# Performance work log

Measured on AMD Instinct MI355X. Metric: run time of the kernel, lower is better.

Reference implementation:

```python
import jax, jax.numpy as jnp
import numpy as np
from jax import lax

# Hyperparameters (match init_kwargs)
B, DIM, H, W = 8, 384, 32, 32
HEADS = 8
GROUPS = 4
OFF_SCALE = 4
K1, K2 = 5, 11  # generate_offset_kernel_sizes(4) -> [5, 11]
OFF_DIM = DIM // GROUPS  # 96
HEAD_DIM = DIM // HEADS  # 48
DN = ('NCHW', 'OIHW', 'NCHW')


def setup_inputs() -> dict:
    key = jax.random.key(0)
    ks = jax.random.split(key, 9)
    std = 0.02
    return {
        'x': jax.random.normal(ks[0], (B, DIM, H, W), jnp.float32),
        'Wq': jax.random.normal(ks[1], (DIM, DIM), jnp.float32) * std,
        'Wk': jax.random.normal(ks[2], (DIM, DIM), jnp.float32) * std,
        'Wv': jax.random.normal(ks[3], (DIM, DIM), jnp.float32) * std,
        'Wproj': jax.random.normal(ks[4], (DIM, DIM), jnp.float32) * std,
        'bproj': jnp.zeros((DIM,), jnp.float32),
        'scale': jnp.ones((1, HEADS, 1, 1), jnp.float32) / np.sqrt(HEAD_DIM),
        'Woff1': jax.random.normal(ks[5], (2, OFF_DIM, K1, K1), jnp.float32) * std,
        'Woff2': jax.random.normal(ks[6], (2, OFF_DIM, K2, K2), jnp.float32) * std,
    }


def _group(t, b, h, w):
    # 'b (h w) (g c) -> (b g) c h w'
    cg = t.shape[-1] // GROUPS
    return t.reshape(b, h, w, GROUPS, cg).transpose(0, 3, 4, 1, 2).reshape(b * GROUPS, cg, h, w)


def _ungroup(t, b, h, w):
    # '(b g) c h w -> b (h w) (g c)'
    cg = t.shape[1]
    return t.reshape(b, GROUPS, cg, h, w).transpose(0, 3, 4, 1, 2).reshape(b, h * w, GROUPS * cg)


def _bilinear(img, ys, xs):
    # img: (c, h, w); ys, xs: (h, w) absolute pixel coords -> (c, h, w)
    h, w = img.shape[1], img.shape[2]
    ys = jnp.clip(ys, 0.0, h - 1.0)
    xs = jnp.clip(xs, 0.0, w - 1.0)
    y0 = jnp.floor(ys); x0 = jnp.floor(xs)
    y0i = y0.astype(jnp.int32); x0i = x0.astype(jnp.int32)
    y1i = jnp.minimum(y0i + 1, h - 1); x1i = jnp.minimum(x0i + 1, w - 1)
    wy = ys - y0; wx = xs - x0
    g = lambda yi, xi: img[:, yi, xi]  # (c, h, w) gather
    return (g(y0i, x0i) * (1 - wy) * (1 - wx) + g(y0i, x1i) * (1 - wy) * wx
            + g(y1i, x0i) * wy * (1 - wx) + g(y1i, x1i) * wy * wx)


def reference(x, Wq, Wk, Wv, Wproj, bproj, scale, Woff1, Woff2):
    b, c, h, w = x.shape
    n = h * w
    xt = x.reshape(b, c, n).transpose(0, 2, 1)  # b n c
    q = xt @ Wq.T  # b n c

    # Offset generator: per-group multi-scale convs -> tanh-bounded offsets scaled by offset_scale
    qg = _group(q, b, h, w)  # (b*g, off_dim, h, w)
    off = (lax.conv_general_dilated(qg, Woff1, (1, 1), 'SAME', dimension_numbers=DN)
           + lax.conv_general_dilated(qg, Woff2, (1, 1), 'SAME', dimension_numbers=DN))
    offsets = jnp.tanh(off) * OFF_SCALE  # (b*g, 2, h, w)

    # apply_offsets: bilinear gather of grouped x at base grid + offsets
    xg = _group(xt, b, h, w)  # (b*g, off_dim, h, w)
    by, bx = jnp.meshgrid(jnp.arange(h, dtype=jnp.float32), jnp.arange(w, dtype=jnp.float32), indexing='ij')
    ys = by[None] + offsets[:, 0]
    xs = bx[None] + offsets[:, 1]
    kv = jax.vmap(_bilinear)(xg, ys, xs)  # (b*g, off_dim, h, w)
    kvf = _ungroup(kv, b, h, w)  # b n c

    k = kvf @ Wk.T
    v = kvf @ Wv.T
    heads = lambda t: t.reshape(b, n, HEADS, HEAD_DIM).transpose(0, 2, 1, 3)  # b h n d
    qh, kh, vh = heads(q), heads(k), heads(v)

    attn = jnp.einsum('bhid,bhjd->bhij', qh, kh) * scale  # learnable per-head scale
    attn = jax.nn.softmax(attn, axis=-1)
    out = jnp.einsum('bhij,bhjd->bhid', attn, vh)  # b h n d
    out = out.transpose(0, 2, 1, 3).reshape(b, n, c)
    out = out @ Wproj.T + bproj
    return out.transpose(0, 2, 1).reshape(b, c, h, w)
```

## Files before the change

### kernel.cpp

```cpp
#include <hip/hip_runtime.h>
#include <hip/hip_bf16.h>

#define DIMC 384
#define NHEADS 8
#define HDIM 48
#define OFFD 96
#define NPIX 1024
#define BB 8

typedef short bf16s;
typedef __attribute__((ext_vector_type(8))) short short8;
typedef __attribute__((ext_vector_type(4))) float f32x4;

__device__ __forceinline__ short f2b(float f) {
  union { float f; unsigned u; } v; v.f = f;
  unsigned r = (v.u + 0x7fffu + ((v.u >> 16) & 1u)) >> 16;
  return (short)r;
}
__device__ __forceinline__ float b2f(short s) {
  union { unsigned u; float f; } v; v.u = ((unsigned)(unsigned short)s) << 16; return v.f;
}
__device__ __forceinline__ unsigned pk2(float a, float b) {
  union { __hip_bfloat162 h; unsigned u; } v;
  v.h = __float22bfloat162_rn(float2{a, b});
  return v.u;
}

__global__ __launch_bounds__(256) void prep_weights(
    const float* __restrict__ Wq, const float* __restrict__ Wk,
    const float* __restrict__ Wv, const float* __restrict__ Wp,
    bf16s* __restrict__ wqh, bf16s* __restrict__ wql,
    bf16s* __restrict__ wkb, bf16s* __restrict__ wvb, bf16s* __restrict__ wpb) {
  int idx = blockIdx.x * 256 + threadIdx.x;
  if (idx >= 4 * 147456) return;
  int which = idx / 147456, e = idx % 147456;
  if (which == 0) {
    float v = Wq[e]; short h = f2b(v);
    wqh[e] = h; wql[e] = f2b(v - b2f(h));
  } else if (which == 1) wkb[e] = f2b(Wk[e]);
  else if (which == 2) wvb[e] = f2b(Wv[e]);
  else wpb[e] = f2b(Wp[e]);
}

__global__ __launch_bounds__(256) void transpose_split(const float* __restrict__ x,
    bf16s* __restrict__ xh, bf16s* __restrict__ xl) {
  __shared__ float ts[64][65];
  int np0 = blockIdx.x * 64, c0 = blockIdx.y * 64, b = blockIdx.z;
  int t = threadIdx.x;
  int a = t & 63, bq = t >> 6;
#pragma unroll
  for (int i = 0; i < 16; ++i) {
    int cl = bq + i * 4;
    ts[cl][a] = x[((size_t)(b * DIMC + c0 + cl)) * NPIX + np0 + a];
  }
  __syncthreads();
#pragma unroll
  for (int i = 0; i < 16; ++i) {
    int npl = bq + i * 4;
    float v = ts[a][npl];
    short h = f2b(v);
    size_t o = ((size_t)(b * NPIX + np0 + npl)) * DIMC + c0 + a;
    xh[o] = h; xl[o] = f2b(v - b2f(h));
  }
}

template<int MODE>
__global__ __launch_bounds__(256) void gemm_lds(
    const bf16s* __restrict__ Ah, const bf16s* __restrict__ Al,
    const bf16s* __restrict__ Wa, const bf16s* __restrict__ Wb,
    float* __restrict__ outF, bf16s* __restrict__ outB, bf16s* __restrict__ outB2,
    const float* __restrict__ bias) {
  __shared__ __align__(16) short wlds[25600];
  const int NS  = (MODE == 2) ? 1 : 2;
  const int KCN = (MODE == 2) ? 48 : 24;
  const int STR = (MODE == 2) ? 392 : 200;
  int t = threadIdx.x;
  int w = t >> 6, lane = t & 63, quad = lane >> 4, l16 = lane & 15;
  int n0 = blockIdx.x * 64;
  int m0 = blockIdx.y * 64 + w * 16;
  f32x4 acc[4], acc2[4];
#pragma unroll
  for (int nt = 0; nt < 4; ++nt) {
    acc[nt] = (f32x4){0.f, 0.f, 0.f, 0.f};
    if (MODE != 2) acc2[nt] = (f32x4){0.f, 0.f, 0.f, 0.f};
  }
  const bf16s* arow_a = Ah + (size_t)(m0 + l16) * DIMC;
  const bf16s* arow_l = (MODE == 0) ? (Al + (size_t)(m0 + l16) * DIMC) : nullptr;

  for (int s = 0; s < NS; ++s) {
    if (s) __syncthreads();
    int kcb = s * 24;
#pragma unroll
    for (int ii = 0; ii < (KCN * 64) / 256; ++ii) {
      int i = ii * 256 + t;
      int n = i / KCN, kcl = i % KCN;
      *(short8*)(&wlds[n * STR + kcl * 8]) =
          *(const short8*)(Wa + (size_t)(n0 + n) * DIMC + (kcb + kcl) * 8);
      if (MODE != 2)
        *(short8*)(&wlds[12800 + n * STR + kcl * 8]) =
            *(const short8*)(Wb + (size_t)(n0 + n) * DIMC + (kcb + kcl) * 8);
    }
    __syncthreads();
    int k0beg = s * 6, k0cnt = (MODE == 2) ? 12 : 6;
#pragma unroll
    for (int kk = 0; kk < k0cnt; ++kk) {
      int k0 = k0beg + kk;
      short8 a0 = *(const short8*)(arow_a + k0 * 32 + quad * 8);
      short8 a1;
      if (MODE == 0) a1 = *(const short8*)(arow_l + k0 * 32 + quad * 8);
      int kcl = kk * 4 + quad;
#pragma unroll
      for (int nt = 0; nt < 4; ++nt) {
        int n = nt * 16 + l16;
        short8 b0 = *(const short8*)(&wlds[n * STR + kcl * 8]);
        acc[nt] = __builtin_amdgcn_mfma_f32_16x16x32_bf16(a0, b0, acc[nt], 0, 0, 0);
        if (MODE == 0) {
          short8 b1 = *(const short8*)(&wlds[12800 + n * STR + kcl * 8]);
          acc[nt] = __builtin_amdgcn_mfma_f32_16x16x32_bf16(a1, b0, acc[nt], 0, 0, 0);
          acc[nt] = __builtin_amdgcn_mfma_f32_16x16x32_bf16(a0, b1, acc[nt], 0, 0, 0);
        } else if (MODE == 1) {
          short8 b1 = *(const short8*)(&wlds[12800 + n * STR + kcl * 8]);
          acc2[nt] = __builtin_amdgcn_mfma_f32_16x16x32_bf16(a0, b1, acc2[nt], 0, 0, 0);
        }
      }
    }
  }
#pragma unroll
  for (int nt = 0; nt < 4; ++nt) {
    int c = n0 + nt * 16 + l16;
#pragma unroll
    for (int r = 0; r < 4; ++r) {
      int m = m0 + quad * 4 + r;
      int b = m >> 10, np = m & 1023;
      float v = acc[nt][r];
      if (MODE == 0) {
        int g = c / OFFD, cc = c % OFFD;
        outF[((size_t)((b * 4 + g) * OFFD + cc)) * NPIX + np] = v;
        int h = c / HDIM, d = c % HDIM;
        outB[((size_t)((b * 8 + h) * NPIX + np)) * 64 + d] = f2b(v);
      } else if (MODE == 1) {
        int h = c / HDIM, d = c % HDIM;
        outB[((size_t)((b * 8 + h) * NPIX + np)) * 64 + d] = f2b(v);
        outB2[((size_t)((b * 8 + h) * HDIM + d)) * NPIX + np] = f2b(acc2[nt][r]);
      } else {
        outF[((size_t)(b * DIMC + c)) * NPIX + np] = v + bias[c];
      }
    }
  }
}

__global__ __launch_bounds__(256) void conv_off_part(const float* __restrict__ qg,
    const float* __restrict__ W1, const float* __restrict__ W2, float* __restrict__ pbuf) {
  __shared__ float ts[42 * 43];
  int chunk = blockIdx.x & 15, bg = blockIdx.x >> 4;
  int t = threadIdx.x;
  int y = t >> 3, x0 = (t & 7) * 4;
  float a0[4] = {0.f, 0.f, 0.f, 0.f}, a1[4] = {0.f, 0.f, 0.f, 0.f};
  const float* plane0 = qg + (size_t)bg * OFFD * NPIX;
  for (int ci = 0; ci < 6; ++ci) {
    int cc = chunk * 6 + ci;
    const float* plane = plane0 + (size_t)cc * NPIX;
    __syncthreads();
    for (int e = t; e < 42 * 42; e += 256) {
      int r = e / 42, c = e - r * 42;
      int gy = r - 5, gx = c - 5;
      ts[r * 43 + c] = (gy >= 0 && gy < 32 && gx >= 0 && gx < 32) ? plane[gy * 32 + gx] : 0.f;
    }
    __syncthreads();
    const float* w1c0 = W1 + (size_t)cc * 25;
    const float* w1c1 = W1 + (size_t)(OFFD + cc) * 25;
    const float* w2c0 = W2 + (size_t)cc * 121;
    const float* w2c1 = W2 + (size_t)(OFFD + cc) * 121;
#pragma unroll
    for (int ky = 0; ky < 11; ++ky) {
      float rv[14];
#pragma unroll
      for (int j = 0; j < 14; ++j) rv[j] = ts[(y + ky) * 43 + x0 + j];
#pragma unroll
      for (int kx = 0; kx < 11; ++kx) {
        float w0 = w2c0[ky * 11 + kx], w1v = w2c1[ky * 11 + kx];
#pragma unroll
        for (int o = 0; o < 4; ++o) {
          a0[o] = fmaf(rv[kx + o], w0, a0[o]);
          a1[o] = fmaf(rv[kx + o], w1v, a1[o]);
        }
      }
    }
#pragma unroll
    for (int ky = 0; ky < 5; ++ky) {
      float rv[8];
#pragma unroll
      for (int j = 0; j < 8; ++j) rv[j] = ts[(y + ky + 3) * 43 + x0 + 3 + j];
#pragma unroll
      for (int kx = 0; kx < 5; ++kx) {
        float w0 = w1c0[ky * 5 + kx], w1v = w1c1[ky * 5 + kx];
#pragma unroll
        for (int o = 0; o < 4; ++o) {
          a0[o] = fmaf(rv[kx + o], w0, a0[o]);
          a1[o] = fmaf(rv[kx + o], w1v, a1[o]);
        }
      }
    }
  }
  float* pb = pbuf + ((size_t)(chunk * 32 + bg) * 2) * NPIX;
#pragma unroll
  for (int o = 0; o < 4; ++o) {
    int n = y * 32 + x0 + o;
    pb[n] = a0[o];
    pb[NPIX + n] = a1[o];
  }
}

__global__ __launch_bounds__(256) void conv_off_reduce(const float* __restrict__ pbuf,
                                                       float* __restrict__ offs) {
  int idx = blockIdx.x * 256 + threadIdx.x;
  float s = 0.f;
#pragma unroll
  for (int ch = 0; ch < 16; ++ch) s += pbuf[(size_t)ch * 65536 + idx];
  offs[idx] = tanhf(s) * 4.0f;
}

__global__ __launch_bounds__(256) void bilinear_kernel(const float* __restrict__ x,
    const float* __restrict__ offs, bf16s* __restrict__ kvf) {
  int chunk = blockIdx.x & 7, ntile = (blockIdx.x >> 3) & 3, bg = blockIdx.x >> 5;
  int n = ntile * 256 + threadIdx.x;
  int b = bg >> 2, g = bg & 3;
  int iy = n >> 5, ix = n & 31;
  float ys = (float)iy + offs[(size_t)bg * 2 * NPIX + n];
  float xs = (float)ix + offs[(size_t)bg * 2 * NPIX + NPIX + n];
  ys = fminf(fmaxf(ys, 0.f), 31.f);
  xs = fminf(fmaxf(xs, 0.f), 31.f);
  float y0f = floorf(ys), x0f = floorf(xs);
  int y0 = (int)y0f, x0 = (int)x0f;
  int y1 = min(y0 + 1, 31), x1 = min(x0 + 1, 31);
  float wy = ys - y0f, wx = xs - x0f;
  float w00 = (1.f - wy) * (1.f - wx), w01 = (1.f - wy) * wx;
  float w10 = wy * (1.f - wx), w11 = wy * wx;
  const float* xp = x + ((size_t)b * DIMC + g * OFFD + chunk * 12) * NPIX;
  bf16s* out = kvf + (size_t)(b * 1024 + n) * DIMC + g * OFFD + chunk * 12;
  int i00 = y0 * 32 + x0, i01 = y0 * 32 + x1, i10 = y1 * 32 + x0, i11 = y1 * 32 + x1;
#pragma unroll
  for (int cc = 0; cc < 12; ++cc) {
    const float* pl = xp + (size_t)cc * NPIX;
    out[cc] = f2b(w00 * pl[i00] + w01 * pl[i01] + w10 * pl[i10] + w11 * pl[i11]);
  }
}

__global__ __launch_bounds__(256, 8) void flash_attn_kernel(
    const bf16s* __restrict__ qb, const bf16s* __restrict__ kb,
    const bf16s* __restrict__ vt, const float* __restrict__ scale,
    bf16s* __restrict__ out) {
  __shared__ short Ps[4][16 * 140];
  int tid = threadIdx.x;
  int w = tid >> 6, lane = tid & 63;
  int quad = lane >> 4, l16 = lane & 15;
  int bh = blockIdx.x & 63, qt32 = blockIdx.x >> 6;
  int b = bh >> 3, h = bh & 7;
  int q0 = qt32 * 32 + (w & 1) * 16;
  int khalf = w >> 1;
  float sc = scale[h] * 1.44269504f;

  const bf16s* qbase = qb + (size_t)bh * NPIX * 64;
  const bf16s* kbase = kb + (size_t)bh * NPIX * 64;
  const bf16s* vbase = vt + (size_t)bh * HDIM * NPIX;

  short8 bq0, bq1;
  {
    const bf16s* qrow = qbase + (size_t)(q0 + l16) * 64;
    short8 r0 = *(const short8*)(qrow + quad * 8);
    short8 r1 = *(const short8*)(qrow + 32 + quad * 8);
#pragma unroll
    for (int j = 0; j < 8; ++j) {
      bq0[j] = f2b(b2f(r0[j]) * sc);
      bq1[j] = f2b(b2f(r1[j]) * sc);
    }
  }
  float l_run = 0.f;
  f32x4 O[3];
#pragma unroll
  for (int nt = 0; nt < 3; ++nt) O[nt] = (f32x4){0.f, 0.f, 0.f, 0.f};
  short* ps = &Ps[w][0];

#pragma unroll 1
  for (int kt = 0; kt < 4; ++kt) {
    int key0 = khalf * 512 + kt * 128;
    f32x4 Sv[8];
#pragma unroll
    for (int s = 0; s < 2; ++s)
#pragma unroll
      for (int nt = 0; nt < 4; ++nt) {
        const bf16s* krow = kbase + (size_t)(key0 + s * 64 + nt * 16 + l16) * 64;
        short8 ak0 = *(const short8*)(krow + quad * 8);
        short8 ak1 = *(const short8*)(krow + 32 + quad * 8);
        f32x4 acc = (f32x4){0.f, 0.f, 0.f, 0.f};
        acc = __builtin_amdgcn_mfma_f32_16x16x32_bf16(ak0, bq0, acc, 0, 0, 0);
        acc = __builtin_amdgcn_mfma_f32_16x16x32_bf16(ak1, bq1, acc, 0, 0, 0);
        Sv[s * 4 + nt] = acc;
      }
    float ls0 = 0.f, ls1 = 0.f, ls2 = 0.f, ls3 = 0.f;
#pragma unroll
    for (int i = 0; i < 8; i += 4) {
#pragma unroll
      for (int r = 0; r < 4; ++r) {
        float p0 = __builtin_amdgcn_exp2f(Sv[i][r]);
        float p1 = __builtin_amdgcn_exp2f(Sv[i + 1][r]);
        float p2 = __builtin_amdgcn_exp2f(Sv[i + 2][r]);
        float p3 = __builtin_amdgcn_exp2f(Sv[i + 3][r]);
        Sv[i][r] = p0; Sv[i + 1][r] = p1; Sv[i + 2][r] = p2; Sv[i + 3][r] = p3;
        ls0 += p0; ls1 += p1; ls2 += p2; ls3 += p3;
      }
    }
    float ls = (ls0 + ls1) + (ls2 + ls3);
    ls += __shfl_xor(ls, 16, 64);
    ls += __shfl_xor(ls, 32, 64);
    l_run += ls;
#pragma unroll
    for (int s = 0; s < 2; ++s)
#pragma unroll
      for (int nt = 0; nt < 4; ++nt) {
        uint2 pk;
        pk.x = pk2(Sv[s * 4 + nt][0], Sv[s * 4 + nt][1]);
        pk.y = pk2(Sv[s * 4 + nt][2], Sv[s * 4 + nt][3]);
        *(uint2*)(ps + l16 * 140 + s * 64 + nt * 16 + quad * 4) = pk;
      }
#pragma unroll
    for (int ks = 0; ks < 4; ++ks) {
      short8 ap = *(short8*)(ps + l16 * 140 + ks * 32 + quad * 8);
#pragma unroll
      for (int nt = 0; nt < 3; ++nt) {
        const bf16s* vrow = vbase + (size_t)(nt * 16 + l16) * NPIX + key0 + ks * 32;
        short8 bv = *(const short8*)(vrow + quad * 8);
        O[nt] = __builtin_amdgcn_mfma_f32_16x16x32_bf16(ap, bv, O[nt], 0, 0, 0);
      }
    }
  }
  if (w >= 2) {
    float* xb = (float*)ps;
#pragma unroll
    for (int nt = 0; nt < 3; ++nt)
#pragma unroll
      for (int r = 0; r < 4; ++r) xb[lane * 13 + nt * 4 + r] = O[nt][r];
    xb[lane * 13 + 12] = l_run;
  }
  __syncthreads();
  if (w < 2) {
    const float* src = (const float*)&Ps[w + 2][0];
#pragma unroll
    for (int nt = 0; nt < 3; ++nt)
#pragma unroll
      for (int r = 0; r < 4; ++r) O[nt][r] += src[lane * 13 + nt * 4 + r];
    l_run += src[lane * 13 + 12];
#pragma unroll
    for (int r = 0; r < 4; ++r) {
      float lr = __shfl(l_run, quad * 4 + r, 64);
      float inv = 1.0f / lr;
      int qrow = q0 + quad * 4 + r;
      bf16s* orow = out + ((size_t)(b * 1024 + qrow)) * DIMC + h * HDIM;
#pragma unroll
      for (int nt = 0; nt < 3; ++nt) orow[nt * 16 + l16] = f2b(O[nt][r] * inv);
    }
  }
}

extern "C" void kernel_launch(void* const* d_in, const int* in_sizes, int n_in,
                              void* d_out, int out_size, void* d_ws, size_t ws_size,
                              hipStream_t stream) {
  const float* x  = (const float*)d_in[0];
  const float* Wq = (const float*)d_in[1];
  const float* Wk = (const float*)d_in[2];
  const float* Wv = (const float*)d_in[3];
  const float* Wp = (const float*)d_in[4];
  const float* bp = (const float*)d_in[5];
  const float* sc = (const float*)d_in[6];
  const float* W1 = (const float*)d_in[7];
  const float* W2 = (const float*)d_in[8];
  float* ws = (float*)d_ws;
  const size_t S = (size_t)BB * NPIX * DIMC;
  const size_t SP = (size_t)64 * NPIX * 64;
  float* qg   = ws;
  float* offs = ws + S;
  float* pbuf = ws + S + 65536;
  bf16s* sb   = (bf16s*)(ws + S + 65536 + 1048576);
  bf16s* xh   = sb;
  bf16s* xl   = sb + S;
  bf16s* qbuf = sb + 2 * S;
  bf16s* kvfb = qbuf + SP;
  bf16s* vbuf = kvfb + S;
  bf16s* wqh  = vbuf + S;
  bf16s* wql  = wqh + 147456;
  bf16s* wkb  = wql + 147456;
  bf16s* wvb  = wkb + 147456;
  bf16s* wpb  = wvb + 147456;
  bf16s* attnout = (bf16s*)qg;
  bf16s* kbuf = xh;

  hipMemsetAsync(qbuf, 0, SP * sizeof(bf16s), stream);
  prep_weights<<<2304, 256, 0, stream>>>(Wq, Wk, Wv, Wp, wqh, wql, wkb, wvb, wpb);
  transpose_split<<<dim3(16, 6, BB), 256, 0, stream>>>(x, xh, xl);
  gemm_lds<0><<<dim3(6, 128), 256, 0, stream>>>(xh, xl, wqh, wql, qg, qbuf, nullptr, nullptr);
  hipMemsetAsync(kbuf, 0, SP * sizeof(bf16s), stream);
  conv_off_part<<<512, 256, 0, stream>>>(qg, W1, W2, pbuf);
  conv_off_reduce<<<256, 256, 0, stream>>>(pbuf, offs);
  bilinear_kernel<<<1024, 256, 0, stream>>>(x, offs, kvfb);
  gemm_lds<1><<<dim3(6, 128), 256, 0, stream>>>(kvfb, nullptr, wkb, wvb, nullptr, kbuf, vbuf, nullptr);
  flash_attn_kernel<<<2048, 256, 0, stream>>>(qbuf, kbuf, vbuf, sc, attnout);
  gemm_lds<2><<<dim3(6, 128), 256, 0, stream>>>(attnout, nullptr, wpb, nullptr, (float*)d_out, nullptr, nullptr, bp);
}
```

Measured before the change: 307.1 us.

## Restructure flash attention to full-key waves and batch conv channel loads

The attention kernel now gives each wave 16 queries and all 1024 keys, with 64 queries per block and half as many blocks. This removes the cross-wave LDS reduction, the barrier and the per-tile row-sum shuffles. The P tile in LDS is double-buffered and V fragments are prefetched one k-step ahead to overlap loads with MFMAs, and the occupancy hint in launch bounds is dropped. The offset convolution stages two channel planes per barrier pair instead of one, halving the synchronisations at the cost of more LDS. The risks are longer per-wave serial work, lower parallelism and possible register pressure without the occupancy hint.

Result: faster. 299.9 us (-2.3%).

```diff
diff --git a/kernel.cpp b/kernel.cpp
--- a/kernel.cpp
+++ b/kernel.cpp
@@ -151,53 +151,59 @@
 
 __global__ __launch_bounds__(256) void conv_off_part(const float* __restrict__ qg,
     const float* __restrict__ W1, const float* __restrict__ W2, float* __restrict__ pbuf) {
-  __shared__ float ts[42 * 43];
+  __shared__ float ts[2][42 * 43];
   int chunk = blockIdx.x & 15, bg = blockIdx.x >> 4;
   int t = threadIdx.x;
   int y = t >> 3, x0 = (t & 7) * 4;
   float a0[4] = {0.f, 0.f, 0.f, 0.f}, a1[4] = {0.f, 0.f, 0.f, 0.f};
   const float* plane0 = qg + (size_t)bg * OFFD * NPIX;
-  for (int ci = 0; ci < 6; ++ci) {
-    int cc = chunk * 6 + ci;
-    const float* plane = plane0 + (size_t)cc * NPIX;
+  for (int ci2 = 0; ci2 < 3; ++ci2) {
+    int ccb = chunk * 6 + ci2 * 2;
     __syncthreads();
-    for (int e = t; e < 42 * 42; e += 256) {
-      int r = e / 42, c = e - r * 42;
+    for (int e = t; e < 2 * 42 * 42; e += 256) {
+      int u = e >= 42 * 42;
+      int e2 = e - u * 42 * 42;
+      int r = e2 / 42, c = e2 - r * 42;
       int gy = r - 5, gx = c - 5;
-      ts[r * 43 + c] = (gy >= 0 && gy < 32 && gx >= 0 && gx < 32) ? plane[gy * 32 + gx] : 0.f;
+      const float* plane = plane0 + (size_t)(ccb + u) * NPIX;
+      ts[u][r * 43 + c] = (gy >= 0 && gy < 32 && gx >= 0 && gx < 32) ? plane[gy * 32 + gx] : 0.f;
     }
     __syncthreads();
-    const float* w1c0 = W1 + (size_t)cc * 25;
-    const float* w1c1 = W1 + (size_t)(OFFD + cc) * 25;
-    const float* w2c0 = W2 + (size_t)cc * 121;
-    const float* w2c1 = W2 + (size_t)(OFFD + cc) * 121;
-#pragma unroll
-    for (int ky = 0; ky < 11; ++ky) {
-      float rv[14];
-#pragma unroll
-      for (int j = 0; j < 14; ++j) rv[j] = ts[(y + ky) * 43 + x0 + j];
-#pragma unroll
-      for (int kx = 0; kx < 11; ++kx) {
-        float w0 = w2c0[ky * 11 + kx], w1v = w2c1[ky * 11 + kx];
-#pragma unroll
-        for (int o = 0; o < 4; ++o) {
-          a0[o] = fmaf(rv[kx + o], w0, a0[o]);
-          a1[o] = fmaf(rv[kx + o], w1v, a1[o]);
+#pragma unroll
+    for (int u = 0; u < 2; ++u) {
+      int cc = ccb + u;
+      const float* w1c0 = W1 + (size_t)cc * 25;
+      const float* w1c1 = W1 + (size_t)(OFFD + cc) * 25;
+      const float* w2c0 = W2 + (size_t)cc * 121;
+      const float* w2c1 = W2 + (size_t)(OFFD + cc) * 121;
+#pragma unroll
+      for (int ky = 0; ky < 11; ++ky) {
+        float rv[14];
+#pragma unroll
+        for (int j = 0; j < 14; ++j) rv[j] = ts[u][(y + ky) * 43 + x0 + j];
+#pragma unroll
+        for (int kx = 0; kx < 11; ++kx) {
+          float w0 = w2c0[ky * 11 + kx], w1v = w2c1[ky * 11 + kx];
+#pragma unroll
+          for (int o = 0; o < 4; ++o) {
+            a0[o] = fmaf(rv[kx + o], w0, a0[o]);
+            a1[o] = fmaf(rv[kx + o], w1v, a1[o]);
+          }
         }
       }
-    }
-#pragma unroll
-    for (int ky = 0; ky < 5; ++ky) {
-      float rv[8];
-#pragma unroll
-      for (int j = 0; j < 8; ++j) rv[j] = ts[(y + ky + 3) * 43 + x0 + 3 + j];
-#pragma unroll
-      for (int kx = 0; kx < 5; ++kx) {
-        float w0 = w1c0[ky * 5 + kx], w1v = w1c1[ky * 5 + kx];
-#pragma unroll
-        for (int o = 0; o < 4; ++o) {
-          a0[o] = fmaf(rv[kx + o], w0, a0[o]);
-          a1[o] = fmaf(rv[kx + o], w1v, a1[o]);
+#pragma unroll
+      for (int ky = 0; ky < 5; ++ky) {
+        float rv[8];
+#pragma unroll
+        for (int j = 0; j < 8; ++j) rv[j] = ts[u][(y + ky + 3) * 43 + x0 + 3 + j];
+#pragma unroll
+        for (int kx = 0; kx < 5; ++kx) {
+          float w0 = w1c0[ky * 5 + kx], w1v = w1c1[ky * 5 + kx];
+#pragma unroll
+          for (int o = 0; o < 4; ++o) {
+            a0[o] = fmaf(rv[kx + o], w0, a0[o]);
+            a1[o] = fmaf(rv[kx + o], w1v, a1[o]);
+          }
         }
       }
     }
@@ -246,18 +252,17 @@
   }
 }
 
-__global__ __launch_bounds__(256, 8) void flash_attn_kernel(
+__global__ __launch_bounds__(256) void flash_attn_kernel(
     const bf16s* __restrict__ qb, const bf16s* __restrict__ kb,
     const bf16s* __restrict__ vt, const float* __restrict__ scale,
     bf16s* __restrict__ out) {
-  __shared__ short Ps[4][16 * 140];
+  __shared__ short Ps[4][2][16 * 140];
   int tid = threadIdx.x;
   int w = tid >> 6, lane = tid & 63;
   int quad = lane >> 4, l16 = lane & 15;
-  int bh = blockIdx.x & 63, qt32 = blockIdx.x >> 6;
+  int qt = blockIdx.x >> 6, bh = blockIdx.x & 63;
   int b = bh >> 3, h = bh & 7;
-  int q0 = qt32 * 32 + (w & 1) * 16;
-  int khalf = w >> 1;
+  int q0 = qt * 64 + w * 16;
   float sc = scale[h] * 1.44269504f;
 
   const bf16s* qbase = qb + (size_t)bh * NPIX * 64;
@@ -279,11 +284,11 @@
   f32x4 O[3];
 #pragma unroll
   for (int nt = 0; nt < 3; ++nt) O[nt] = (f32x4){0.f, 0.f, 0.f, 0.f};
-  short* ps = &Ps[w][0];
-
-#pragma unroll 1
-  for (int kt = 0; kt < 4; ++kt) {
-    int key0 = khalf * 512 + kt * 128;
+
+#pragma unroll 2
+  for (int kt = 0; kt < 8; ++kt) {
+    int key0 = kt * 128;
+    short* ps = &Ps[w][kt & 1][0];
     f32x4 Sv[8];
 #pragma unroll
     for (int s = 0; s < 2; ++s)
@@ -310,10 +315,7 @@
         ls0 += p0; ls1 += p1; ls2 += p2; ls3 += p3;
       }
     }
-    float ls = (ls0 + ls1) + (ls2 + ls3);
-    ls += __shfl_xor(ls, 16, 64);
-    ls += __shfl_xor(ls, 32, 64);
-    l_run += ls;
+    l_run += (ls0 + ls1) + (ls2 + ls3);
 #pragma unroll
     for (int s = 0; s < 2; ++s)
 #pragma unroll
@@ -323,42 +325,38 @@
         pk.y = pk2(Sv[s * 4 + nt][2], Sv[s * 4 + nt][3]);
         *(uint2*)(ps + l16 * 140 + s * 64 + nt * 16 + quad * 4) = pk;
       }
+    short8 bv[3];
+#pragma unroll
+    for (int nt = 0; nt < 3; ++nt)
+      bv[nt] = *(const short8*)(vbase + (size_t)(nt * 16 + l16) * NPIX + key0 + quad * 8);
 #pragma unroll
     for (int ks = 0; ks < 4; ++ks) {
       short8 ap = *(short8*)(ps + l16 * 140 + ks * 32 + quad * 8);
-#pragma unroll
-      for (int nt = 0; nt < 3; ++nt) {
-        const bf16s* vrow = vbase + (size_t)(nt * 16 + l16) * NPIX + key0 + ks * 32;
-        short8 bv = *(const short8*)(vrow + quad * 8);
-        O[nt] = __builtin_amdgcn_mfma_f32_16x16x32_bf16(ap, bv, O[nt], 0, 0, 0);
-      }
-    }
-  }
-  if (w >= 2) {
-    float* xb = (float*)ps;
-#pragma unroll
-    for (int nt = 0; nt < 3; ++nt)
-#pragma unroll
-      for (int r = 0; r < 4; ++r) xb[lane * 13 + nt * 4 + r] = O[nt][r];
-    xb[lane * 13 + 12] = l_run;
-  }
-  __syncthreads();
-  if (w < 2) {
-    const float* src = (const float*)&Ps[w + 2][0];
-#pragma unroll
-    for (int nt = 0; nt < 3; ++nt)
-#pragma unroll
-      for (int r = 0; r < 4; ++r) O[nt][r] += src[lane * 13 + nt * 4 + r];
-    l_run += src[lane * 13 + 12];
-#pragma unroll
-    for (int r = 0; r < 4; ++r) {
-      float lr = __shfl(l_run, quad * 4 + r, 64);
-      float inv = 1.0f / lr;
-      int qrow = q0 + quad * 4 + r;
-      bf16s* orow = out + ((size_t)(b * 1024 + qrow)) * DIMC + h * HDIM;
-#pragma unroll
-      for (int nt = 0; nt < 3; ++nt) orow[nt * 16 + l16] = f2b(O[nt][r] * inv);
-    }
+      short8 bvn[3];
+      if (ks < 3) {
+#pragma unroll
+        for (int nt = 0; nt < 3; ++nt)
+          bvn[nt] = *(const short8*)(vbase + (size_t)(nt * 16 + l16) * NPIX + key0 + (ks + 1) * 32 + quad * 8);
+      }
+#pragma unroll
+      for (int nt = 0; nt < 3; ++nt)
+        O[nt] = __builtin_amdgcn_mfma_f32_16x16x32_bf16(ap, bv[nt], O[nt], 0, 0, 0);
+      if (ks < 3) {
+#pragma unroll
+        for (int nt = 0; nt < 3; ++nt) bv[nt] = bvn[nt];
+      }
+    }
+  }
+  l_run += __shfl_xor(l_run, 16, 64);
+  l_run += __shfl_xor(l_run, 32, 64);
+#pragma unroll
+  for (int r = 0; r < 4; ++r) {
+    float lr = __shfl(l_run, quad * 4 + r, 64);
+    float inv = 1.0f / lr;
+    int qrow = q0 + quad * 4 + r;
+    bf16s* orow = out + ((size_t)(b * 1024 + qrow)) * DIMC + h * HDIM;
+#pragma unroll
+    for (int nt = 0; nt < 3; ++nt) orow[nt * 16 + l16] = f2b(O[nt][r] * inv);
   }
 }
 
@@ -403,6 +401,6 @@
   conv_off_reduce<<<256, 256, 0, stream>>>(pbuf, offs);
   bilinear_kernel<<<1024, 256, 0, stream>>>(x, offs, kvfb);
   gemm_lds<1><<<dim3(6, 128), 256, 0, stream>>>(kvfb, nullptr, wkb, wvb, nullptr, kbuf, vbuf, nullptr);
-  flash_attn_kernel<<<2048, 256, 0, stream>>>(qbuf, kbuf, vbuf, sc, attnout);
+  flash_attn_kernel<<<1024, 256, 0, stream>>>(qbuf, kbuf, vbuf, sc, attnout);
   gemm_lds<2><<<dim3(6, 128), 256, 0, stream>>>(attnout, nullptr, wpb, nullptr, (float*)d_out, nullptr, nullptr, bp);
 }
```
